# Optimization experiments

Measured on AMD Instinct MI355X. Metric: run time of the kernel, lower is better.

Reference implementation:

```python
import jax, jax.numpy as jnp
import numpy as np

# Fuzzy-logic decoder: rules = [[0,0,0],[1,0,1]] (hardcoded in the torch module's __init__).
# For each rule [p, a, b] firing on predicate p:
#   num[s,o] = max_k min(t[a, s, k], t[b, k, o])   (max-min relation composition)
# amalgamate(x, y) = x + y - x*y (probabilistic OR); new starts at 0, and
# amalgamate(x, 0) = x, so with exactly one rule per predicate:
#   t_new[p] = amalgamate(t[p], num_p) = t[p] + num_p - t[p]*num_p

def _compose(A, B):
    # A: [S, K], B: [K, O] -> max over k of elementwise min -> [S, O]
    return jnp.max(jnp.minimum(A[:, :, None], B[None, :, :]), axis=1)


def setup_inputs() -> dict:
    key = jax.random.key(0)
    t = jax.random.uniform(key, (2, 512, 512), dtype=jnp.float32)
    return {"t": t}


def reference(t) -> jnp.ndarray:
    t0, t1 = t[0], t[1]
    num0 = _compose(t0, t0)          # rule [0,0,0]
    num1 = _compose(t0, t1)          # rule [1,0,1]
    num = jnp.stack([num0, num1], axis=0)  # [2, S, O]
    return t + num - t * num         # amalgamate(t, num)
```

## Files before the change

kernel.cpp:

```cpp
#include <hip/hip_runtime.h>


#define SDIM 512
#define TS 32
#define TO 32
#define BK 64
#define BK2 32
#define NCH (SDIM / BK)
#define BSTR 36

typedef _Float16 h2 __attribute__((ext_vector_type(2)));

__device__ __forceinline__ h2 pack2(float a, float b) {
    return __builtin_bit_cast(h2, __builtin_amdgcn_cvt_pkrtz(a, b));
}
__device__ __forceinline__ h2 pmin(h2 a, h2 b) { return __builtin_elementwise_min(a, b); }
__device__ __forceinline__ h2 pmax(h2 a, h2 b) { return __builtin_elementwise_max(a, b); }
__device__ __forceinline__ h2 bch2(unsigned u) { return __builtin_bit_cast(h2, u); }

__global__ __launch_bounds__(256, 2) void fuzzy_compose_kernel(
        const float* __restrict__ t, float* __restrict__ out) {
    __shared__ h2 AlsT[BK2][TS];
    __shared__ h2 Bls[BK2][BSTR];

    const int tid = threadIdx.x;
    const int o0 = blockIdx.x * TO;
    const int s0 = blockIdx.y * TS;
    const int p  = blockIdx.z;

    const float* __restrict__ B = t + p * (SDIM * SDIM);

    const int ol = (tid & 15) * 2, sl = (tid >> 4) * 2;
    const int ar = tid >> 3, aq = tid & 7;
    const int acol = ar ^ (aq << 2);
    const int bk2 = tid >> 3, bq = tid & 7;

    const float4* __restrict__ Arow =
        reinterpret_cast<const float4*>(t + (s0 + ar) * SDIM);

    h2 acc[2][2];
    acc[0][0] = pack2(0.f, 0.f); acc[0][1] = pack2(0.f, 0.f);
    acc[1][0] = pack2(0.f, 0.f); acc[1][1] = pack2(0.f, 0.f);

    float4 fa0, fa1, fx, fy;
    fa0 = Arow[aq * 2 + 0];
    fa1 = Arow[aq * 2 + 1];
    fx = *reinterpret_cast<const float4*>(B + (2 * bk2) * SDIM + o0 + bq * 4);
    fy = *reinterpret_cast<const float4*>(B + (2 * bk2 + 1) * SDIM + o0 + bq * 4);

    for (int c = 0; c < NCH; ++c) {
        {
            const int k2b = aq * 4;
            AlsT[k2b + 0][acol] = pack2(fa0.x, fa0.y);
            AlsT[k2b + 1][acol] = pack2(fa0.z, fa0.w);
            AlsT[k2b + 2][acol] = pack2(fa1.x, fa1.y);
            AlsT[k2b + 3][acol] = pack2(fa1.z, fa1.w);
            uint4 u;
            u.x = __builtin_bit_cast(unsigned, pack2(fx.x, fy.x));
            u.y = __builtin_bit_cast(unsigned, pack2(fx.y, fy.y));
            u.z = __builtin_bit_cast(unsigned, pack2(fx.z, fy.z));
            u.w = __builtin_bit_cast(unsigned, pack2(fx.w, fy.w));
            *reinterpret_cast<uint4*>(&Bls[bk2][bq * 4]) = u;
        }
        __syncthreads();

        if (c + 1 < NCH) {
            const int k0 = (c + 1) * BK;
            fa0 = Arow[k0 / 4 + aq * 2 + 0];
            fa1 = Arow[k0 / 4 + aq * 2 + 1];
            fx = *reinterpret_cast<const float4*>(B + (k0 + 2 * bk2) * SDIM + o0 + bq * 4);
            fy = *reinterpret_cast<const float4*>(B + (k0 + 2 * bk2 + 1) * SDIM + o0 + bq * 4);
        }

        #pragma unroll
        for (int k2 = 0; k2 < BK2; ++k2) {
            const int swz = ((k2 >> 2) & 7) << 2;
            const uint2 ua = *reinterpret_cast<const uint2*>(&AlsT[k2][sl ^ swz]);
            const uint2 ub = *reinterpret_cast<const uint2*>(&Bls[k2][ol]);
            const h2 a0 = bch2(ua.x), a1 = bch2(ua.y);
            const h2 b0 = bch2(ub.x), b1 = bch2(ub.y);
            acc[0][0] = pmax(acc[0][0], pmin(a0, b0));
            acc[0][1] = pmax(acc[0][1], pmin(a0, b1));
            acc[1][0] = pmax(acc[1][0], pmin(a1, b0));
            acc[1][1] = pmax(acc[1][1], pmin(a1, b1));
        }
        __syncthreads();
    }

    const float* __restrict__ tp = t + p * (SDIM * SDIM);
    float* __restrict__ op = out + p * (SDIM * SDIM);
    #pragma unroll
    for (int j = 0; j < 2; ++j) {
        const int row = s0 + sl + j;
        const float2 tv = *reinterpret_cast<const float2*>(tp + row * SDIM + o0 + ol);
        const float n0 = fmaxf((float)acc[j][0][0], (float)acc[j][0][1]);
        const float n1 = fmaxf((float)acc[j][1][0], (float)acc[j][1][1]);
        float2 r;
        r.x = tv.x + n0 - tv.x * n0;
        r.y = tv.y + n1 - tv.y * n1;
        *reinterpret_cast<float2*>(op + row * SDIM + o0 + ol) = r;
    }
}

extern "C" void kernel_launch(void* const* d_in, const int* in_sizes, int n_in,
                              void* d_out, int out_size, void* d_ws, size_t ws_size,
                              hipStream_t stream) {
    const float* t = (const float*)d_in[0];
    float* out = (float*)d_out;
    dim3 grid(SDIM / TO, SDIM / TS, 2);
    fuzzy_compose_kernel<<<grid, 256, 0, stream>>>(t, out);
}
```

Baseline: 69.56 us.

## Split K across blocks with wider output tiles and a separate combine kernel

The K reduction is split into two halves handled by separate blocks. Each half writes its fp16 partial max into the output buffer as interleaved halves, and a second kernel takes the max of the two and applies the amalgamate step. The output tile widens to 64 columns, so each thread holds a 2x4 accumulator block. The old XOR swizzle on A is replaced by padded strides. Together this raises per-thread reuse and keeps the grid size the same. The cost is an extra kernel launch and an extra round trip through global memory.

```diff
diff --git a/kernel.cpp b/kernel.cpp
--- a/kernel.cpp
+++ b/kernel.cpp
@@ -3,11 +3,13 @@
 
 #define SDIM 512
 #define TS 32
-#define TO 32
+#define TO 64
+#define KHALF 256
 #define BK 64
 #define BK2 32
-#define NCH (SDIM / BK)
-#define BSTR 36
+#define NCH (KHALF / BK)
+#define ASTR 34
+#define BSTR 68
 
 typedef _Float16 h2 __attribute__((ext_vector_type(2)));
 
@@ -17,89 +19,133 @@
 __device__ __forceinline__ h2 pmin(h2 a, h2 b) { return __builtin_elementwise_min(a, b); }
 __device__ __forceinline__ h2 pmax(h2 a, h2 b) { return __builtin_elementwise_max(a, b); }
 __device__ __forceinline__ h2 bch2(unsigned u) { return __builtin_bit_cast(h2, u); }
+__device__ __forceinline__ unsigned bcu(h2 v) { return __builtin_bit_cast(unsigned, v); }
 
-__global__ __launch_bounds__(256, 2) void fuzzy_compose_kernel(
+__global__ __launch_bounds__(256, 2) void compose_partial(
         const float* __restrict__ t, float* __restrict__ out) {
-    __shared__ h2 AlsT[BK2][TS];
+    __shared__ h2 Als[BK2][ASTR];
     __shared__ h2 Bls[BK2][BSTR];
 
     const int tid = threadIdx.x;
     const int o0 = blockIdx.x * TO;
     const int s0 = blockIdx.y * TS;
-    const int p  = blockIdx.z;
+    const int p  = blockIdx.z >> 1;
+    const int kh = blockIdx.z & 1;
+    const int kb = kh * KHALF;
 
     const float* __restrict__ B = t + p * (SDIM * SDIM);
 
-    const int ol = (tid & 15) * 2, sl = (tid >> 4) * 2;
+    const int ol = (tid & 15) * 4;
+    const int sl = (tid >> 4) * 2;
     const int ar = tid >> 3, aq = tid & 7;
-    const int acol = ar ^ (aq << 2);
     const int bk2 = tid >> 3, bq = tid & 7;
 
     const float4* __restrict__ Arow =
         reinterpret_cast<const float4*>(t + (s0 + ar) * SDIM);
 
-    h2 acc[2][2];
-    acc[0][0] = pack2(0.f, 0.f); acc[0][1] = pack2(0.f, 0.f);
-    acc[1][0] = pack2(0.f, 0.f); acc[1][1] = pack2(0.f, 0.f);
+    h2 acc[2][4];
+    #pragma unroll
+    for (int j = 0; j < 2; ++j)
+        #pragma unroll
+        for (int i = 0; i < 4; ++i) acc[j][i] = pack2(0.f, 0.f);
 
-    float4 fa0, fa1, fx, fy;
-    fa0 = Arow[aq * 2 + 0];
-    fa1 = Arow[aq * 2 + 1];
-    fx = *reinterpret_cast<const float4*>(B + (2 * bk2) * SDIM + o0 + bq * 4);
-    fy = *reinterpret_cast<const float4*>(B + (2 * bk2 + 1) * SDIM + o0 + bq * 4);
+    float4 fa0, fa1, fx, fx2, fy, fy2;
+    {
+        const int kf = kb / 4 + aq * 2;
+        fa0 = Arow[kf];
+        fa1 = Arow[kf + 1];
+        const float* __restrict__ Bb = B + (kb + 2 * bk2) * SDIM + o0 + bq * 8;
+        fx  = *reinterpret_cast<const float4*>(Bb);
+        fx2 = *reinterpret_cast<const float4*>(Bb + 4);
+        fy  = *reinterpret_cast<const float4*>(Bb + SDIM);
+        fy2 = *reinterpret_cast<const float4*>(Bb + SDIM + 4);
+    }
 
     for (int c = 0; c < NCH; ++c) {
         {
             const int k2b = aq * 4;
-            AlsT[k2b + 0][acol] = pack2(fa0.x, fa0.y);
-            AlsT[k2b + 1][acol] = pack2(fa0.z, fa0.w);
-            AlsT[k2b + 2][acol] = pack2(fa1.x, fa1.y);
-            AlsT[k2b + 3][acol] = pack2(fa1.z, fa1.w);
-            uint4 u;
-            u.x = __builtin_bit_cast(unsigned, pack2(fx.x, fy.x));
-            u.y = __builtin_bit_cast(unsigned, pack2(fx.y, fy.y));
-            u.z = __builtin_bit_cast(unsigned, pack2(fx.z, fy.z));
-            u.w = __builtin_bit_cast(unsigned, pack2(fx.w, fy.w));
-            *reinterpret_cast<uint4*>(&Bls[bk2][bq * 4]) = u;
+            Als[k2b + 0][ar] = pack2(fa0.x, fa0.y);
+            Als[k2b + 1][ar] = pack2(fa0.z, fa0.w);
+            Als[k2b + 2][ar] = pack2(fa1.x, fa1.y);
+            Als[k2b + 3][ar] = pack2(fa1.z, fa1.w);
+            uint4 u0, u1;
+            u0.x = bcu(pack2(fx.x, fy.x));
+            u0.y = bcu(pack2(fx.y, fy.y));
+            u0.z = bcu(pack2(fx.z, fy.z));
+            u0.w = bcu(pack2(fx.w, fy.w));
+            u1.x = bcu(pack2(fx2.x, fy2.x));
+            u1.y = bcu(pack2(fx2.y, fy2.y));
+            u1.z = bcu(pack2(fx2.z, fy2.z));
+            u1.w = bcu(pack2(fx2.w, fy2.w));
+            *reinterpret_cast<uint4*>(&Bls[bk2][bq * 8]) = u0;
+            *reinterpret_cast<uint4*>(&Bls[bk2][bq * 8 + 4]) = u1;
         }
         __syncthreads();
 
         if (c + 1 < NCH) {
-            const int k0 = (c + 1) * BK;
-            fa0 = Arow[k0 / 4 + aq * 2 + 0];
-            fa1 = Arow[k0 / 4 + aq * 2 + 1];
-            fx = *reinterpret_cast<const float4*>(B + (k0 + 2 * bk2) * SDIM + o0 + bq * 4);
-            fy = *reinterpret_cast<const float4*>(B + (k0 + 2 * bk2 + 1) * SDIM + o0 + bq * 4);
+            const int k0 = kb + (c + 1) * BK;
+            const int kf = k0 / 4 + aq * 2;
+            fa0 = Arow[kf];
+            fa1 = Arow[kf + 1];
+            const float* __restrict__ Bb = B + (k0 + 2 * bk2) * SDIM + o0 + bq * 8;
+            fx  = *reinterpret_cast<const float4*>(Bb);
+            fx2 = *reinterpret_cast<const float4*>(Bb + 4);
+            fy  = *reinterpret_cast<const float4*>(Bb + SDIM);
+            fy2 = *reinterpret_cast<const float4*>(Bb + SDIM + 4);
         }
 
         #pragma unroll
         for (int k2 = 0; k2 < BK2; ++k2) {
-            const int swz = ((k2 >> 2) & 7) << 2;
-            const uint2 ua = *reinterpret_cast<const uint2*>(&AlsT[k2][sl ^ swz]);
-            const uint2 ub = *reinterpret_cast<const uint2*>(&Bls[k2][ol]);
+            const uint2 ua = *reinterpret_cast<const uint2*>(&Als[k2][sl]);
+            const uint4 ub = *reinterpret_cast<const uint4*>(&Bls[k2][ol]);
             const h2 a0 = bch2(ua.x), a1 = bch2(ua.y);
             const h2 b0 = bch2(ub.x), b1 = bch2(ub.y);
+            const h2 b2 = bch2(ub.z), b3 = bch2(ub.w);
             acc[0][0] = pmax(acc[0][0], pmin(a0, b0));
             acc[0][1] = pmax(acc[0][1], pmin(a0, b1));
+            acc[0][2] = pmax(acc[0][2], pmin(a0, b2));
+            acc[0][3] = pmax(acc[0][3], pmin(a0, b3));
             acc[1][0] = pmax(acc[1][0], pmin(a1, b0));
             acc[1][1] = pmax(acc[1][1], pmin(a1, b1));
+            acc[1][2] = pmax(acc[1][2], pmin(a1, b2));
+            acc[1][3] = pmax(acc[1][3], pmin(a1, b3));
         }
         __syncthreads();
     }
 
-    const float* __restrict__ tp = t + p * (SDIM * SDIM);
-    float* __restrict__ op = out + p * (SDIM * SDIM);
+    unsigned short* __restrict__ op = reinterpret_cast<unsigned short*>(out);
     #pragma unroll
     for (int j = 0; j < 2; ++j) {
         const int row = s0 + sl + j;
-        const float2 tv = *reinterpret_cast<const float2*>(tp + row * SDIM + o0 + ol);
-        const float n0 = fmaxf((float)acc[j][0][0], (float)acc[j][0][1]);
-        const float n1 = fmaxf((float)acc[j][1][0], (float)acc[j][1][1]);
-        float2 r;
-        r.x = tv.x + n0 - tv.x * n0;
-        r.y = tv.y + n1 - tv.y * n1;
-        *reinterpret_cast<float2*>(op + row * SDIM + o0 + ol) = r;
+        #pragma unroll
+        for (int i = 0; i < 4; ++i) {
+            const int o = o0 + ol + i;
+            const float nm = fmaxf((float)acc[j][i][0], (float)acc[j][i][1]);
+            const _Float16 hh = (_Float16)nm;
+            op[(((p * SDIM) + row) * SDIM + o) * 2 + kh] =
+                __builtin_bit_cast(unsigned short, hh);
+        }
     }
+}
+
+__global__ __launch_bounds__(256) void combine_amalg(
+        const float* __restrict__ t, float* __restrict__ out) {
+    const int idx = blockIdx.x * 256 + threadIdx.x;
+    const uint4 w = reinterpret_cast<const uint4*>(out)[idx];
+    const float4 tv = reinterpret_cast<const float4*>(t)[idx];
+    const unsigned wv[4] = {w.x, w.y, w.z, w.w};
+    const float tf[4] = {tv.x, tv.y, tv.z, tv.w};
+    float rs[4];
+    #pragma unroll
+    for (int i = 0; i < 4; ++i) {
+        const _Float16 h0 = __builtin_bit_cast(_Float16, (unsigned short)(wv[i] & 0xffffu));
+        const _Float16 h1 = __builtin_bit_cast(_Float16, (unsigned short)(wv[i] >> 16));
+        const float num = fmaxf((float)h0, (float)h1);
+        rs[i] = tf[i] + num - tf[i] * num;
+    }
+    float4 r;
+    r.x = rs[0]; r.y = rs[1]; r.z = rs[2]; r.w = rs[3];
+    reinterpret_cast<float4*>(out)[idx] = r;
 }
 
 extern "C" void kernel_launch(void* const* d_in, const int* in_sizes, int n_in,
@@ -107,6 +153,7 @@
                               hipStream_t stream) {
     const float* t = (const float*)d_in[0];
     float* out = (float*)d_out;
-    dim3 grid(SDIM / TO, SDIM / TS, 2);
-    fuzzy_compose_kernel<<<grid, 256, 0, stream>>>(t, out);
+    dim3 g1(SDIM / TO, SDIM / TS, 4);
+    compose_partial<<<g1, 256, 0, stream>>>(t, out);
+    combine_amalg<<<dim3(512), 256, 0, stream>>>(t, out);
 }
```

Measured after the change: 71.43 us. 2.7% more time.

## Stage the full K dimension in LDS with one load phase and single barrier

Applied to the files above, without the earlier changes.

Replaces the 8-chunk double-buffered K loop with one bulk load: each thread issues all of its global loads for the whole 512-long K range up front, converts them to packed fp16, writes the entire A and B tiles into LDS, then runs a single 256-step max-min loop after one barrier. This removes the per-chunk synchronisation and lets all global loads be in flight at once. In exchange it uses 64KB of LDS per block and many more live registers (16+16 float4s). That may limit occupancy under the 2-blocks-per-CU launch bound, and the loads no longer overlap with compute. The A-tile swizzle is also dropped, so LDS bank conflicts may appear.

```diff
diff --git a/kernel.cpp b/kernel.cpp
--- a/kernel.cpp
+++ b/kernel.cpp
@@ -4,10 +4,7 @@
 #define SDIM 512
 #define TS 32
 #define TO 32
-#define BK 64
-#define BK2 32
-#define NCH (SDIM / BK)
-#define BSTR 36
+#define K2N 256
 
 typedef _Float16 h2 __attribute__((ext_vector_type(2)));
 
@@ -17,82 +14,78 @@
 __device__ __forceinline__ h2 pmin(h2 a, h2 b) { return __builtin_elementwise_min(a, b); }
 __device__ __forceinline__ h2 pmax(h2 a, h2 b) { return __builtin_elementwise_max(a, b); }
 __device__ __forceinline__ h2 bch2(unsigned u) { return __builtin_bit_cast(h2, u); }
+__device__ __forceinline__ unsigned bcu(h2 v) { return __builtin_bit_cast(unsigned, v); }
 
-__global__ __launch_bounds__(256, 2) void fuzzy_compose_kernel(
+__global__ __launch_bounds__(256, 2) void fuzzy_fused(
         const float* __restrict__ t, float* __restrict__ out) {
-    __shared__ h2 AlsT[BK2][TS];
-    __shared__ h2 Bls[BK2][BSTR];
+    __shared__ h2 Als[K2N][TS];
+    __shared__ h2 Bls[K2N][TO];
 
     const int tid = threadIdx.x;
     const int o0 = blockIdx.x * TO;
     const int s0 = blockIdx.y * TS;
     const int p  = blockIdx.z;
 
-    const float* __restrict__ B = t + p * (SDIM * SDIM);
+    const float* __restrict__ Bp = t + p * (SDIM * SDIM);
 
-    const int ol = (tid & 15) * 2, sl = (tid >> 4) * 2;
     const int ar = tid >> 3, aq = tid & 7;
-    const int acol = ar ^ (aq << 2);
-    const int bk2 = tid >> 3, bq = tid & 7;
-
     const float4* __restrict__ Arow =
         reinterpret_cast<const float4*>(t + (s0 + ar) * SDIM);
+    float4 fa[16];
+    #pragma unroll
+    for (int j = 0; j < 16; ++j) fa[j] = Arow[aq + 8 * j];
+
+    const int bq = tid & 7, bp = tid >> 3;
+    const float* __restrict__ Bb = Bp + o0 + bq * 4;
+    float4 fx[8], fy[8];
+    #pragma unroll
+    for (int j = 0; j < 8; ++j) {
+        const int r2 = (bp + 32 * j) * 2;
+        fx[j] = *reinterpret_cast<const float4*>(Bb + r2 * SDIM);
+        fy[j] = *reinterpret_cast<const float4*>(Bb + (r2 + 1) * SDIM);
+    }
+
+    #pragma unroll
+    for (int j = 0; j < 16; ++j) {
+        const int k2b = 2 * (aq + 8 * j);
+        Als[k2b    ][ar] = pack2(fa[j].x, fa[j].y);
+        Als[k2b + 1][ar] = pack2(fa[j].z, fa[j].w);
+    }
+    #pragma unroll
+    for (int j = 0; j < 8; ++j) {
+        uint4 u;
+        u.x = bcu(pack2(fx[j].x, fy[j].x));
+        u.y = bcu(pack2(fx[j].y, fy[j].y));
+        u.z = bcu(pack2(fx[j].z, fy[j].z));
+        u.w = bcu(pack2(fx[j].w, fy[j].w));
+        *reinterpret_cast<uint4*>(&Bls[bp + 32 * j][bq * 4]) = u;
+    }
+    __syncthreads();
+
+    const int ol = (tid & 15) * 2;
+    const int sl = (tid >> 4) * 2;
 
     h2 acc[2][2];
     acc[0][0] = pack2(0.f, 0.f); acc[0][1] = pack2(0.f, 0.f);
     acc[1][0] = pack2(0.f, 0.f); acc[1][1] = pack2(0.f, 0.f);
 
-    float4 fa0, fa1, fx, fy;
-    fa0 = Arow[aq * 2 + 0];
-    fa1 = Arow[aq * 2 + 1];
-    fx = *reinterpret_cast<const float4*>(B + (2 * bk2) * SDIM + o0 + bq * 4);
-    fy = *reinterpret_cast<const float4*>(B + (2 * bk2 + 1) * SDIM + o0 + bq * 4);
-
-    for (int c = 0; c < NCH; ++c) {
-        {
-            const int k2b = aq * 4;
-            AlsT[k2b + 0][acol] = pack2(fa0.x, fa0.y);
-            AlsT[k2b + 1][acol] = pack2(fa0.z, fa0.w);
-            AlsT[k2b + 2][acol] = pack2(fa1.x, fa1.y);
-            AlsT[k2b + 3][acol] = pack2(fa1.z, fa1.w);
-            uint4 u;
-            u.x = __builtin_bit_cast(unsigned, pack2(fx.x, fy.x));
-            u.y = __builtin_bit_cast(unsigned, pack2(fx.y, fy.y));
-            u.z = __builtin_bit_cast(unsigned, pack2(fx.z, fy.z));
-            u.w = __builtin_bit_cast(unsigned, pack2(fx.w, fy.w));
-            *reinterpret_cast<uint4*>(&Bls[bk2][bq * 4]) = u;
-        }
-        __syncthreads();
-
-        if (c + 1 < NCH) {
-            const int k0 = (c + 1) * BK;
-            fa0 = Arow[k0 / 4 + aq * 2 + 0];
-            fa1 = Arow[k0 / 4 + aq * 2 + 1];
-            fx = *reinterpret_cast<const float4*>(B + (k0 + 2 * bk2) * SDIM + o0 + bq * 4);
-            fy = *reinterpret_cast<const float4*>(B + (k0 + 2 * bk2 + 1) * SDIM + o0 + bq * 4);
-        }
-
-        #pragma unroll
-        for (int k2 = 0; k2 < BK2; ++k2) {
-            const int swz = ((k2 >> 2) & 7) << 2;
-            const uint2 ua = *reinterpret_cast<const uint2*>(&AlsT[k2][sl ^ swz]);
-            const uint2 ub = *reinterpret_cast<const uint2*>(&Bls[k2][ol]);
-            const h2 a0 = bch2(ua.x), a1 = bch2(ua.y);
-            const h2 b0 = bch2(ub.x), b1 = bch2(ub.y);
-            acc[0][0] = pmax(acc[0][0], pmin(a0, b0));
-            acc[0][1] = pmax(acc[0][1], pmin(a0, b1));
-            acc[1][0] = pmax(acc[1][0], pmin(a1, b0));
-            acc[1][1] = pmax(acc[1][1], pmin(a1, b1));
-        }
-        __syncthreads();
+    #pragma unroll 8
+    for (int k2 = 0; k2 < K2N; ++k2) {
+        const uint2 ua = *reinterpret_cast<const uint2*>(&Als[k2][sl]);
+        const uint2 ub = *reinterpret_cast<const uint2*>(&Bls[k2][ol]);
+        const h2 a0 = bch2(ua.x), a1 = bch2(ua.y);
+        const h2 b0 = bch2(ub.x), b1 = bch2(ub.y);
+        acc[0][0] = pmax(acc[0][0], pmin(a0, b0));
+        acc[0][1] = pmax(acc[0][1], pmin(a0, b1));
+        acc[1][0] = pmax(acc[1][0], pmin(a1, b0));
+        acc[1][1] = pmax(acc[1][1], pmin(a1, b1));
     }
 
-    const float* __restrict__ tp = t + p * (SDIM * SDIM);
     float* __restrict__ op = out + p * (SDIM * SDIM);
     #pragma unroll
     for (int j = 0; j < 2; ++j) {
         const int row = s0 + sl + j;
-        const float2 tv = *reinterpret_cast<const float2*>(tp + row * SDIM + o0 + ol);
+        const float2 tv = *reinterpret_cast<const float2*>(Bp + row * SDIM + o0 + ol);
         const float n0 = fmaxf((float)acc[j][0][0], (float)acc[j][0][1]);
         const float n1 = fmaxf((float)acc[j][1][0], (float)acc[j][1][1]);
         float2 r;
@@ -108,5 +101,5 @@
     const float* t = (const float*)d_in[0];
     float* out = (float*)d_out;
     dim3 grid(SDIM / TO, SDIM / TS, 2);
-    fuzzy_compose_kernel<<<grid, 256, 0, stream>>>(t, out);
+    fuzzy_fused<<<grid, 256, 0, stream>>>(t, out);
 }
```

New measurement: 70.42 us. About the same (+1.2%).
